# Performance work log

Hardware: AMD Instinct MI355X
Metric: run time of the kernel (lower is better)

## Reference

```python
import jax, jax.numpy as jnp
from jax import lax
import numpy as np

B, C, H, W = 2, 64, 128, 128
DN = ('NCHW', 'OIHW', 'NCHW')


def setup_inputs() -> dict:
    key = jax.random.key(0)
    ks = jax.random.split(key, 20)
    rn = lambda k, s, sc=0.05: jax.random.normal(k, s, dtype=jnp.float32) * sc
    inp = {
        'x': jax.random.normal(ks[0], (B, C, H, W), dtype=jnp.float32),
        'off1_w': rn(ks[1], (C, 1, 1, 15)), 'off1_b': rn(ks[2], (C,)),
        'bn1_s': 1.0 + rn(ks[3], (C,)), 'bn1_b': rn(ks[4], (C,)),
        'off2_w': rn(ks[5], (C, 1, 15, 1)), 'off2_b': rn(ks[6], (C,)),
        'bn2_s': 1.0 + rn(ks[7], (C,)), 'bn2_b': rn(ks[8], (C,)),
        'off3_w': rn(ks[9], (C, 1, 3, 3)), 'off3_b': rn(ks[10], (C,)),
        'bn3_s': 1.0 + rn(ks[11], (C,)), 'bn3_b': rn(ks[12], (C,)),
        'bal_w': rn(ks[13], (18, C, 1, 1)), 'bal_b': rn(ks[14], (18,)),
        'bn4_s': 1.0 + rn(ks[15], (18,)), 'bn4_b': rn(ks[16], (18,)),
        'dw2': rn(ks[17], (C, 1, 3, 3), 0.1),
        'dw3': rn(jax.random.fold_in(key, 101), (C, 1, 3, 3), 0.1),
        'dw4': rn(jax.random.fold_in(key, 102), (C, 1, 3, 3), 0.1),
        'dw5': rn(jax.random.fold_in(key, 103), (C, 1, 3, 3), 0.1),
        'fin_w': rn(ks[18], (C, C, 1, 1)), 'fin_b': rn(ks[19], (C,)),
        'bn5_s': 1.0 + rn(jax.random.fold_in(key, 104), (C,)),
        'bn5_b': rn(jax.random.fold_in(key, 105), (C,)),
    }
    return inp


def _dwconv(x, w, pad):
    return lax.conv_general_dilated(x, w, (1, 1), [(pad[0], pad[0]), (pad[1], pad[1])],
                                    dimension_numbers=DN, feature_group_count=x.shape[1])


def _conv1x1(x, w):
    return lax.conv_general_dilated(x, w, (1, 1), 'VALID', dimension_numbers=DN)


def _bias(x, b):
    return x + b[None, :, None, None]


def _bn(x, s, b):  # inference-form BatchNorm folded into per-channel affine
    return x * s[None, :, None, None] + b[None, :, None, None]


def _bilinear(x, py, px):
    # x: [B,C,H,W]; py/px: [B,9,H,W] float sampling coords -> [B,C,9,H,W]
    Bn, Cn, Hn, Wn = x.shape
    y0 = jnp.floor(py)
    x0 = jnp.floor(px)
    wy1 = py - y0  # fractional parts
    wx1 = px - x0
    xf = x.reshape(Bn, Cn, Hn * Wn)

    def gather(yi, xi):
        valid = (yi >= 0) & (yi <= Hn - 1) & (xi >= 0) & (xi <= Wn - 1)
        yc = jnp.clip(yi, 0, Hn - 1).astype(jnp.int32)
        xc = jnp.clip(xi, 0, Wn - 1).astype(jnp.int32)
        idx = (yc * Wn + xc).reshape(Bn, -1)  # [B, 9*H*W]
        v = jax.vmap(lambda f, i: f[:, i])(xf, idx)  # [B,C,9*H*W]
        v = v.reshape(Bn, Cn, 9, Hn, Wn)
        return v * valid[:, None].astype(x.dtype)  # zero padding outside

    g00 = gather(y0, x0)
    g01 = gather(y0, x0 + 1)
    g10 = gather(y0 + 1, x0)
    g11 = gather(y0 + 1, x0 + 1)
    wy1e = wy1[:, None]
    wx1e = wx1[:, None]
    return (g00 * (1 - wy1e) * (1 - wx1e) + g01 * (1 - wy1e) * wx1e
            + g10 * wy1e * (1 - wx1e) + g11 * wy1e * wx1e)


def _deform_dw(x, offsets, w, d):
    # depthwise DeformConv2d: kernel 3x3, stride 1, padding=d, dilation=d, groups=C
    Bn, Cn, Hn, Wn = x.shape
    off = offsets.reshape(Bn, 9, 2, Hn, Wn)  # pairs (dy, dx) per kernel tap, row-major
    ky = (jnp.arange(9) // 3 - 1).astype(x.dtype)  # [-1,-1,-1,0,0,0,1,1,1]
    kx = (jnp.arange(9) % 3 - 1).astype(x.dtype)
    hs = jnp.arange(Hn, dtype=x.dtype)
    ws = jnp.arange(Wn, dtype=x.dtype)
    # output loc h maps to input h - pad + ki*dil = h + (ki-1)*d since pad == dil == d
    py = off[:, :, 0] + (hs[:, None] + d * ky[:, None, None])[None]  # [B,9,H,W]
    px = off[:, :, 1] + (ws[None, :] + d * kx[:, None, None])[None]
    s = _bilinear(x, py, px)  # [B,C,9,H,W]
    return jnp.einsum('bckhw,ck->bchw', s, w.reshape(Cn, 9))


def reference(x, off1_w, off1_b, bn1_s, bn1_b, off2_w, off2_b, bn2_s, bn2_b,
              off3_w, off3_b, bn3_s, bn3_b, bal_w, bal_b, bn4_s, bn4_b,
              dw2, dw3, dw4, dw5, fin_w, fin_b, bn5_s, bn5_b):
    # DirectionOffsets: three depthwise convs + BN, summed, then 1x1 -> 18ch + BN
    o1 = _bn(_bias(_dwconv(x, off1_w, (0, 7)), off1_b), bn1_s, bn1_b)
    o2 = _bn(_bias(_dwconv(x, off2_w, (7, 0)), off2_b), bn2_s, bn2_b)
    o3 = _bn(_bias(_dwconv(x, off3_w, (1, 1)), off3_b), bn3_s, bn3_b)
    off = _bn(_bias(_conv1x1(o1 + o2 + o3, bal_w), bal_b), bn4_s, bn4_b)  # [B,18,H,W]
    # four deformable depthwise convs sharing the offset field
    out = (_deform_dw(x, off, dw2, 2) + _deform_dw(x, off, dw3, 3)
           + _deform_dw(x, off, dw4, 4) + _deform_dw(x, off, dw5, 5))
    out = _bn(_bias(_conv1x1(out, fin_w), fin_b), bn5_s, bn5_b) * x
    return out
```

## Files before the change

### kernel.cpp

```cpp
#include <hip/hip_runtime.h>

#define BB 2
#define CC 64
#define HH 128
#define WW 128
#define HWN (HH*WW)
#define CHW (CC*HWN)

#define BAND_H 8
#define HALO   8
#define NBAND  (HH / BAND_H)
#define LROWS  (BAND_H + 2 * HALO)
#define CPB    2
#define XPAD   8
#define XSTR   (WW + 2 * XPAD)

#define OB_H 16
#define OB_HALO 7
#define OB_ROWS (OB_H + 2 * OB_HALO)
#define OSTR 144

__global__ __launch_bounds__(256) void osum_kernel(const float* __restrict__ x,
    const float* __restrict__ w1, const float* __restrict__ b1, const float* __restrict__ s1, const float* __restrict__ g1,
    const float* __restrict__ w2, const float* __restrict__ b2, const float* __restrict__ s2, const float* __restrict__ g2,
    const float* __restrict__ w3, const float* __restrict__ b3, const float* __restrict__ s3, const float* __restrict__ g3,
    float* __restrict__ osum)
{
    __shared__ float xs[OB_ROWS * OSTR];
    int bid  = blockIdx.x;
    int band = bid & 7;
    int bc   = bid >> 3;
    int c    = bc & (CC - 1);
    int bs   = band * OB_H;
    int r_lo_v = bs - OB_HALO;

    for (int i = threadIdx.x; i < (OB_ROWS * OSTR) / 4; i += 256)
        ((float4*)xs)[i] = make_float4(0.f, 0.f, 0.f, 0.f);
    __syncthreads();

    int gstart = r_lo_v < 0 ? 0 : r_lo_v;
    int gend   = r_lo_v + OB_ROWS; if (gend > HH) gend = HH;
    int nitems = (gend - gstart) * (WW / 4);
    const float* xp = x + (size_t)bc * HWN;
    for (int i = threadIdx.x; i < nitems; i += 256) {
        int r = i >> 5, col4 = i & 31;
        int g = gstart + r;
        int lr = g - r_lo_v;
        ((float4*)xs)[lr * (OSTR / 4) + 2 + col4] = ((const float4*)(xp + g * WW))[col4];
    }
    __syncthreads();

    float W1[15], W2[15], W3[9];
    #pragma unroll
    for (int k = 0; k < 15; ++k) { W1[k] = w1[c * 15 + k]; W2[k] = w2[c * 15 + k]; }
    #pragma unroll
    for (int k = 0; k < 9; ++k) W3[k] = w3[c * 9 + k];
    float bb1 = b1[c], ss1 = s1[c], gg1 = g1[c];
    float bb2 = b2[c], ss2 = s2[c], gg2 = g2[c];
    float bb3 = b3[c], ss3 = s3[c], gg3 = g3[c];

    #pragma unroll
    for (int i = 0; i < (OB_H * WW) / 256; ++i) {
        int p = bs * WW + i * 256 + threadIdx.x;
        int h = p >> 7;
        int w = p & (WW - 1);
        int lr = h - r_lo_v;
        int base = lr * OSTR + XPAD + w;

        float a1 = 0.f;
        #pragma unroll
        for (int k = 0; k < 15; ++k) a1 += xs[base + k - 7] * W1[k];
        float a2 = 0.f;
        #pragma unroll
        for (int k = 0; k < 15; ++k) a2 += xs[base + (k - 7) * OSTR] * W2[k];
        float a3 = 0.f;
        #pragma unroll
        for (int kh = 0; kh < 3; ++kh)
            #pragma unroll
            for (int kw = 0; kw < 3; ++kw)
                a3 += xs[base + (kh - 1) * OSTR + (kw - 1)] * W3[kh * 3 + kw];

        osum[(size_t)bc * HWN + p] = (a1 + bb1) * ss1 + gg1
                                   + (a2 + bb2) * ss2 + gg2
                                   + (a3 + bb3) * ss3 + gg3;
    }
}

__global__ __launch_bounds__(256) void off_kernel(const float* __restrict__ osum,
    const float* __restrict__ balw, const float* __restrict__ balb,
    const float* __restrict__ s4, const float* __restrict__ g4,
    float* __restrict__ off)
{
    __shared__ float ls[CC * 128];
    int bid = blockIdx.x;
    int b   = bid >> 7;
    int hw0 = (bid & 127) * 128;

    const float* src = osum + (size_t)b * CHW + hw0;
    #pragma unroll
    for (int i = 0; i < 8; ++i) {
        int idx = threadIdx.x + i * 256;
        int row = idx >> 5, col4 = idx & 31;
        ((float4*)ls)[row * 32 + col4] = *(const float4*)(src + (size_t)row * HWN + col4 * 4);
    }
    __syncthreads();

    int hw = (threadIdx.x & 63) + ((threadIdx.x >> 6) & 1) * 64;
    int og = __builtin_amdgcn_readfirstlane((int)(threadIdx.x >> 7));

    float acc[9];
    #pragma unroll
    for (int j = 0; j < 9; ++j) acc[j] = 0.f;
    for (int ic = 0; ic < CC; ++ic) {
        float v = ls[ic * 128 + hw];
        #pragma unroll
        for (int j = 0; j < 9; ++j)
            acc[j] += v * balw[(og * 9 + j) * CC + ic];
    }
    #pragma unroll
    for (int j = 0; j < 9; ++j) {
        int oc = og * 9 + j;
        off[(size_t)b * (18 * HWN) + (size_t)oc * HWN + hw0 + hw] =
            (acc[j] + balb[oc]) * s4[oc] + g4[oc];
    }
}

__device__ __forceinline__ float gz(const float* __restrict__ xp, int y, int x) {
    return ((unsigned)y < (unsigned)HH && (unsigned)x < (unsigned)WW) ? xp[y * WW + x] : 0.f;
}

__global__ __launch_bounds__(256) void deform_kernel(
    const float* __restrict__ x,
    const float* __restrict__ off,
    const float* __restrict__ dw2, const float* __restrict__ dw3,
    const float* __restrict__ dw4, const float* __restrict__ dw5,
    float* __restrict__ pre)
{
    __shared__ float xs[LROWS * XSTR * CPB];

    int bid  = blockIdx.x;
    int band = bid & (NBAND - 1);
    int bcp  = bid >> 4;
    int cp   = bcp & 31;
    int b    = bcp >> 5;
    int c0   = cp * CPB;
    int bc0  = b * CC + c0;

    int r_lo_v = band * BAND_H - HALO;

    for (int i = threadIdx.x; i < (LROWS * XSTR * CPB) / 4; i += 256)
        ((float4*)xs)[i] = make_float4(0.f, 0.f, 0.f, 0.f);
    __syncthreads();

    int gstart = r_lo_v < 0 ? 0 : r_lo_v;
    int gend   = r_lo_v + LROWS; if (gend > HH) gend = HH;
    int nitems = (gend - gstart) * (WW / 4);
    const float* xp0 = x + (size_t)bc0 * HWN;
    const float* xp1 = xp0 + HWN;
    for (int i = threadIdx.x; i < nitems; i += 256) {
        int r = i >> 5, col4 = i & 31;
        int g = gstart + r;
        int lr = g - r_lo_v;
        float4 q0 = ((const float4*)(xp0 + g * WW))[col4];
        float4 q1 = ((const float4*)(xp1 + g * WW))[col4];
        ((float4*)xs)[lr * (XSTR / 2) + XPAD / 2 + col4 * 2]     = make_float4(q0.x, q1.x, q0.y, q1.y);
        ((float4*)xs)[lr * (XSTR / 2) + XPAD / 2 + col4 * 2 + 1] = make_float4(q0.z, q1.z, q0.w, q1.w);
    }
    __syncthreads();

    const float2* XS2 = (const float2*)xs;
    const float* offb = off + (size_t)b * (18 * HWN);

    #pragma unroll 1
    for (int chunk = 0; chunk < (BAND_H * WW) / 256; ++chunk) {
        int p = band * (BAND_H * WW) + chunk * 256 + (int)threadIdx.x;
        float hf = (float)(p >> 7);
        float wf = (float)(p & (WW - 1));

        float oy[9], ox[9];
        #pragma unroll
        for (int k = 0; k < 9; ++k) {
            oy[k] = offb[((size_t)(2 * k) << 14) + p];
            ox[k] = offb[((size_t)(2 * k + 1) << 14) + p];
        }

        float acc0 = 0.f, acc1 = 0.f;
        #pragma unroll
        for (int k = 0; k < 9; ++k) {
            const int ky = k / 3 - 1, kx = k % 3 - 1;
            float pyb = oy[k] + hf;
            float pxb = ox[k] + wf;
            float y0f = floorf(pyb), x0f = floorf(pxb);
            float wy = pyb - y0f, wx = pxb - x0f;
            int y0g = (int)y0f, x0g = (int)x0f;
            int y0b = y0g - r_lo_v;
            int x0b = x0g + XPAD;
            float cxa = 1.f - wx, cxb = wx;

            const int dkyLo = (ky < 0) ? -5 : (ky > 0 ? 2 : 0);
            const int dkyHi = (ky < 0) ? -2 : (ky > 0 ? 5 : 0);
            const int dkxLo = (kx < 0) ? -5 : (kx > 0 ? 2 : 0);
            const int dkxHi = (kx < 0) ? -2 : (kx > 0 ? 5 : 0);
            bool ok = (y0b + dkyLo >= 0) & (y0b + dkyHi <= LROWS - 2)
                    & (x0b + dkxLo >= 0) & (x0b + dkxHi <= XSTR - 2);

            if (ok) {
                #pragma unroll
                for (int di = 0; di < 4; ++di) {
                    const int d = di + 2;
                    int f0 = (y0b + d * ky) * XSTR + (x0b + d * kx);
                    float2 a  = XS2[f0],        bq = XS2[f0 + 1];
                    float2 cq = XS2[f0 + XSTR], dq = XS2[f0 + XSTR + 1];
                    float ra0 = cxa * a.x + cxb * bq.x;
                    float rb0 = cxa * cq.x + cxb * dq.x;
                    float ra1 = cxa * a.y + cxb * bq.y;
                    float rb1 = cxa * cq.y + cxb * dq.y;
                    float s0 = ra0 + wy * (rb0 - ra0);
                    float s1 = ra1 + wy * (rb1 - ra1);
                    const float* dwp = (di == 0) ? dw2 : (di == 1) ? dw3 : (di == 2) ? dw4 : dw5;
                    acc0 += s0 * dwp[c0 * 9 + k];
                    acc1 += s1 * dwp[(c0 + 1) * 9 + k];
                }
            } else {
                #pragma unroll
                for (int di = 0; di < 4; ++di) {
                    const int d = di + 2;
                    int yy = y0g + d * ky, xx = x0g + d * kx;
                    float v00 = gz(xp0, yy, xx),     v01 = gz(xp0, yy, xx + 1);
                    float v10 = gz(xp0, yy + 1, xx), v11 = gz(xp0, yy + 1, xx + 1);
                    float u00 = gz(xp1, yy, xx),     u01 = gz(xp1, yy, xx + 1);
                    float u10 = gz(xp1, yy + 1, xx), u11 = gz(xp1, yy + 1, xx + 1);
                    float s0 = (1.f - wy) * (cxa * v00 + cxb * v01) + wy * (cxa * v10 + cxb * v11);
                    float s1 = (1.f - wy) * (cxa * u00 + cxb * u01) + wy * (cxa * u10 + cxb * u11);
                    const float* dwp = (di == 0) ? dw2 : (di == 1) ? dw3 : (di == 2) ? dw4 : dw5;
                    acc0 += s0 * dwp[c0 * 9 + k];
                    acc1 += s1 * dwp[(c0 + 1) * 9 + k];
                }
            }
        }
        pre[((size_t)bc0 << 14) + p]       = acc0;
        pre[((size_t)(bc0 + 1) << 14) + p] = acc1;
    }
}

__global__ __launch_bounds__(256) void final_kernel(const float* __restrict__ pre,
    const float* __restrict__ finw, const float* __restrict__ finb,
    const float* __restrict__ s5, const float* __restrict__ g5,
    const float* __restrict__ x, float* __restrict__ out)
{
    __shared__ float ls[CC * 64];
    int bid = blockIdx.x;
    int b   = bid >> 8;
    int hw0 = (bid & 255) * 64;

    const float* src = pre + (size_t)b * CHW + hw0;
    #pragma unroll
    for (int i = 0; i < 4; ++i) {
        int idx = threadIdx.x + i * 256;
        int row = idx >> 4, col4 = idx & 15;
        ((float4*)ls)[row * 16 + col4] = *(const float4*)(src + (size_t)row * HWN + col4 * 4);
    }
    __syncthreads();

    int hw = threadIdx.x & 63;
    int og = __builtin_amdgcn_readfirstlane((int)(threadIdx.x >> 6));

    float acc[16];
    #pragma unroll
    for (int j = 0; j < 16; ++j) acc[j] = 0.f;
    for (int ic = 0; ic < CC; ++ic) {
        float v = ls[ic * 64 + hw];
        #pragma unroll
        for (int j = 0; j < 16; ++j)
            acc[j] += v * finw[(og * 16 + j) * CC + ic];
    }
    #pragma unroll
    for (int j = 0; j < 16; ++j) {
        int oc = og * 16 + j;
        size_t oidx = ((size_t)(b * CC + oc) << 14) + hw0 + hw;
        out[oidx] = ((acc[j] + finb[oc]) * s5[oc] + g5[oc]) * x[oidx];
    }
}

extern "C" void kernel_launch(void* const* d_in, const int* in_sizes, int n_in,
                              void* d_out, int out_size, void* d_ws, size_t ws_size,
                              hipStream_t stream) {
    const float* x      = (const float*)d_in[0];
    const float* off1_w = (const float*)d_in[1];
    const float* off1_b = (const float*)d_in[2];
    const float* bn1_s  = (const float*)d_in[3];
    const float* bn1_b  = (const float*)d_in[4];
    const float* off2_w = (const float*)d_in[5];
    const float* off2_b = (const float*)d_in[6];
    const float* bn2_s  = (const float*)d_in[7];
    const float* bn2_b  = (const float*)d_in[8];
    const float* off3_w = (const float*)d_in[9];
    const float* off3_b = (const float*)d_in[10];
    const float* bn3_s  = (const float*)d_in[11];
    const float* bn3_b  = (const float*)d_in[12];
    const float* bal_w  = (const float*)d_in[13];
    const float* bal_b  = (const float*)d_in[14];
    const float* bn4_s  = (const float*)d_in[15];
    const float* bn4_b  = (const float*)d_in[16];
    const float* dw2    = (const float*)d_in[17];
    const float* dw3    = (const float*)d_in[18];
    const float* dw4    = (const float*)d_in[19];
    const float* dw5    = (const float*)d_in[20];
    const float* fin_w  = (const float*)d_in[21];
    const float* fin_b  = (const float*)d_in[22];
    const float* bn5_s  = (const float*)d_in[23];
    const float* bn5_b  = (const float*)d_in[24];

    float* ws   = (float*)d_ws;
    float* osum = ws;
    float* off  = ws + (size_t)BB * CHW;
    float* pre  = off + (size_t)BB * 18 * HWN;

    float* out = (float*)d_out;

    osum_kernel<<<BB * CC * (HH / OB_H), 256, 0, stream>>>(x,
        off1_w, off1_b, bn1_s, bn1_b,
        off2_w, off2_b, bn2_s, bn2_b,
        off3_w, off3_b, bn3_s, bn3_b, osum);
    off_kernel<<<BB * (HWN / 128), 256, 0, stream>>>(osum, bal_w, bal_b, bn4_s, bn4_b, off);
    deform_kernel<<<BB * (CC / CPB) * NBAND, 256, 0, stream>>>(x, off, dw2, dw3, dw4, dw5, pre);
    final_kernel<<<BB * (HWN / 64), 256, 0, stream>>>(pre, fin_w, fin_b, bn5_s, bn5_b, x, out);
}
```

Before: 162.6 us.

## Process four channels per block and share bilinear taps across dilations

The deformable depthwise kernel now handles four channels per block, with an interleaved float4 LDS layout, so each offset read and each address computation serves four channels instead of two. For the centre tap, where all four dilations sample the same location, the four weights are pre-summed and a single bilinear sample is taken. For axis-aligned taps, the overlapping samples along a row or column are loaded once into a 5-entry register window and reused across dilations. HALO drops to 7 and launch bounds request 3 blocks per SIMD. Costs are half as many blocks, higher register pressure, and larger LDS per block.

```diff
diff --git a/kernel.cpp b/kernel.cpp
--- a/kernel.cpp
+++ b/kernel.cpp
@@ -8,10 +8,10 @@
 #define CHW (CC*HWN)
 
 #define BAND_H 8
-#define HALO   8
+#define HALO   7
 #define NBAND  (HH / BAND_H)
 #define LROWS  (BAND_H + 2 * HALO)
-#define CPB    2
+#define CPB    4
 #define XPAD   8
 #define XSTR   (WW + 2 * XPAD)
 
@@ -129,27 +129,50 @@
     return ((unsigned)y < (unsigned)HH && (unsigned)x < (unsigned)WW) ? xp[y * WW + x] : 0.f;
 }
 
-__global__ __launch_bounds__(256) void deform_kernel(
+__device__ __forceinline__ float bil_g(const float* __restrict__ xp, int yy, int xx,
+                                       float cxa, float cxb, float wy) {
+    float v00 = gz(xp, yy, xx),     v01 = gz(xp, yy, xx + 1);
+    float v10 = gz(xp, yy + 1, xx), v11 = gz(xp, yy + 1, xx + 1);
+    float ra = cxa * v00 + cxb * v01;
+    float rb = cxa * v10 + cxb * v11;
+    return ra + wy * (rb - ra);
+}
+
+__device__ __forceinline__ void bl4(const float4 a, const float4 b, const float4 c, const float4 d,
+                                    float cxa, float cxb, float wy,
+                                    float w0, float w1, float w2, float w3,
+                                    float (&acc)[4])
+{
+    float ra, rb, s;
+    ra = cxa * a.x + cxb * b.x; rb = cxa * c.x + cxb * d.x; s = ra + wy * (rb - ra); acc[0] += s * w0;
+    ra = cxa * a.y + cxb * b.y; rb = cxa * c.y + cxb * d.y; s = ra + wy * (rb - ra); acc[1] += s * w1;
+    ra = cxa * a.z + cxb * b.z; rb = cxa * c.z + cxb * d.z; s = ra + wy * (rb - ra); acc[2] += s * w2;
+    ra = cxa * a.w + cxb * b.w; rb = cxa * c.w + cxb * d.w; s = ra + wy * (rb - ra); acc[3] += s * w3;
+}
+
+#define DWP(di) ((di) == 0 ? dw2 : (di) == 1 ? dw3 : (di) == 2 ? dw4 : dw5)
+
+__global__ __launch_bounds__(256, 3) void deform_kernel(
     const float* __restrict__ x,
     const float* __restrict__ off,
     const float* __restrict__ dw2, const float* __restrict__ dw3,
     const float* __restrict__ dw4, const float* __restrict__ dw5,
     float* __restrict__ pre)
 {
-    __shared__ float xs[LROWS * XSTR * CPB];
+    __shared__ float4 xs4[LROWS * XSTR];
 
     int bid  = blockIdx.x;
     int band = bid & (NBAND - 1);
     int bcp  = bid >> 4;
-    int cp   = bcp & 31;
-    int b    = bcp >> 5;
+    int cp   = bcp & (CC / CPB - 1);
+    int b    = bcp >> 4;
     int c0   = cp * CPB;
     int bc0  = b * CC + c0;
 
     int r_lo_v = band * BAND_H - HALO;
 
-    for (int i = threadIdx.x; i < (LROWS * XSTR * CPB) / 4; i += 256)
-        ((float4*)xs)[i] = make_float4(0.f, 0.f, 0.f, 0.f);
+    for (int i = threadIdx.x; i < LROWS * XSTR; i += 256)
+        xs4[i] = make_float4(0.f, 0.f, 0.f, 0.f);
     __syncthreads();
 
     int gstart = r_lo_v < 0 ? 0 : r_lo_v;
@@ -157,19 +180,33 @@
     int nitems = (gend - gstart) * (WW / 4);
     const float* xp0 = x + (size_t)bc0 * HWN;
     const float* xp1 = xp0 + HWN;
+    const float* xp2 = xp1 + HWN;
+    const float* xp3 = xp2 + HWN;
     for (int i = threadIdx.x; i < nitems; i += 256) {
         int r = i >> 5, col4 = i & 31;
         int g = gstart + r;
         int lr = g - r_lo_v;
         float4 q0 = ((const float4*)(xp0 + g * WW))[col4];
         float4 q1 = ((const float4*)(xp1 + g * WW))[col4];
-        ((float4*)xs)[lr * (XSTR / 2) + XPAD / 2 + col4 * 2]     = make_float4(q0.x, q1.x, q0.y, q1.y);
-        ((float4*)xs)[lr * (XSTR / 2) + XPAD / 2 + col4 * 2 + 1] = make_float4(q0.z, q1.z, q0.w, q1.w);
-    }
-    __syncthreads();
-
-    const float2* XS2 = (const float2*)xs;
+        float4 q2 = ((const float4*)(xp2 + g * WW))[col4];
+        float4 q3 = ((const float4*)(xp3 + g * WW))[col4];
+        float4* dst = &xs4[lr * XSTR + XPAD + col4 * 4];
+        dst[0] = make_float4(q0.x, q1.x, q2.x, q3.x);
+        dst[1] = make_float4(q0.y, q1.y, q2.y, q3.y);
+        dst[2] = make_float4(q0.z, q1.z, q2.z, q3.z);
+        dst[3] = make_float4(q0.w, q1.w, q2.w, q3.w);
+    }
+    __syncthreads();
+
+    const float4* XS4 = xs4;
     const float* offb = off + (size_t)b * (18 * HWN);
+    const float* xpc[4] = { xp0, xp1, xp2, xp3 };
+
+    float wc[4];
+    #pragma unroll
+    for (int j = 0; j < 4; ++j)
+        wc[j] = dw2[(c0 + j) * 9 + 4] + dw3[(c0 + j) * 9 + 4]
+              + dw4[(c0 + j) * 9 + 4] + dw5[(c0 + j) * 9 + 4];
 
     #pragma unroll 1
     for (int chunk = 0; chunk < (BAND_H * WW) / 256; ++chunk) {
@@ -184,7 +221,7 @@
             ox[k] = offb[((size_t)(2 * k + 1) << 14) + p];
         }
 
-        float acc0 = 0.f, acc1 = 0.f;
+        float acc[4] = {0.f, 0.f, 0.f, 0.f};
         #pragma unroll
         for (int k = 0; k < 9; ++k) {
             const int ky = k / 3 - 1, kx = k % 3 - 1;
@@ -205,41 +242,75 @@
                     & (x0b + dkxLo >= 0) & (x0b + dkxHi <= XSTR - 2);
 
             if (ok) {
-                #pragma unroll
-                for (int di = 0; di < 4; ++di) {
-                    const int d = di + 2;
-                    int f0 = (y0b + d * ky) * XSTR + (x0b + d * kx);
-                    float2 a  = XS2[f0],        bq = XS2[f0 + 1];
-                    float2 cq = XS2[f0 + XSTR], dq = XS2[f0 + XSTR + 1];
-                    float ra0 = cxa * a.x + cxb * bq.x;
-                    float rb0 = cxa * cq.x + cxb * dq.x;
-                    float ra1 = cxa * a.y + cxb * bq.y;
-                    float rb1 = cxa * cq.y + cxb * dq.y;
-                    float s0 = ra0 + wy * (rb0 - ra0);
-                    float s1 = ra1 + wy * (rb1 - ra1);
-                    const float* dwp = (di == 0) ? dw2 : (di == 1) ? dw3 : (di == 2) ? dw4 : dw5;
-                    acc0 += s0 * dwp[c0 * 9 + k];
-                    acc1 += s1 * dwp[(c0 + 1) * 9 + k];
+                if (ky == 0 && kx == 0) {
+                    int f0 = y0b * XSTR + x0b;
+                    float4 a = XS4[f0],        bq = XS4[f0 + 1];
+                    float4 cq = XS4[f0 + XSTR], dq = XS4[f0 + XSTR + 1];
+                    bl4(a, bq, cq, dq, cxa, cxb, wy, wc[0], wc[1], wc[2], wc[3], acc);
+                } else if (ky == 0) {
+                    int cbase = x0b + (kx < 0 ? -5 : 2);
+                    int f0 = y0b * XSTR + cbase, f1 = f0 + XSTR;
+                    float4 top[5], bot[5];
+                    #pragma unroll
+                    for (int j = 0; j < 5; ++j) { top[j] = XS4[f0 + j]; bot[j] = XS4[f1 + j]; }
+                    #pragma unroll
+                    for (int di = 0; di < 4; ++di) {
+                        const int jj = (kx < 0) ? (3 - di) : di;
+                        const float* dwp = DWP(di);
+                        bl4(top[jj], top[jj + 1], bot[jj], bot[jj + 1], cxa, cxb, wy,
+                            dwp[(c0 + 0) * 9 + k], dwp[(c0 + 1) * 9 + k],
+                            dwp[(c0 + 2) * 9 + k], dwp[(c0 + 3) * 9 + k], acc);
+                    }
+                } else if (kx == 0) {
+                    int rbase = y0b + (ky < 0 ? -5 : 2);
+                    float4 L[5], R[5];
+                    #pragma unroll
+                    for (int j = 0; j < 5; ++j) {
+                        int f = (rbase + j) * XSTR + x0b;
+                        L[j] = XS4[f]; R[j] = XS4[f + 1];
+                    }
+                    #pragma unroll
+                    for (int di = 0; di < 4; ++di) {
+                        const int jj = (ky < 0) ? (3 - di) : di;
+                        const float* dwp = DWP(di);
+                        bl4(L[jj], R[jj], L[jj + 1], R[jj + 1], cxa, cxb, wy,
+                            dwp[(c0 + 0) * 9 + k], dwp[(c0 + 1) * 9 + k],
+                            dwp[(c0 + 2) * 9 + k], dwp[(c0 + 3) * 9 + k], acc);
+                    }
+                } else {
+                    #pragma unroll
+                    for (int di = 0; di < 4; ++di) {
+                        const int d = di + 2;
+                        int f0 = (y0b + d * ky) * XSTR + (x0b + d * kx);
+                        float4 a = XS4[f0],        bq = XS4[f0 + 1];
+                        float4 cq = XS4[f0 + XSTR], dq = XS4[f0 + XSTR + 1];
+                        const float* dwp = DWP(di);
+                        bl4(a, bq, cq, dq, cxa, cxb, wy,
+                            dwp[(c0 + 0) * 9 + k], dwp[(c0 + 1) * 9 + k],
+                            dwp[(c0 + 2) * 9 + k], dwp[(c0 + 3) * 9 + k], acc);
+                    }
                 }
             } else {
-                #pragma unroll
-                for (int di = 0; di < 4; ++di) {
-                    const int d = di + 2;
-                    int yy = y0g + d * ky, xx = x0g + d * kx;
-                    float v00 = gz(xp0, yy, xx),     v01 = gz(xp0, yy, xx + 1);
-                    float v10 = gz(xp0, yy + 1, xx), v11 = gz(xp0, yy + 1, xx + 1);
-                    float u00 = gz(xp1, yy, xx),     u01 = gz(xp1, yy, xx + 1);
-                    float u10 = gz(xp1, yy + 1, xx), u11 = gz(xp1, yy + 1, xx + 1);
-                    float s0 = (1.f - wy) * (cxa * v00 + cxb * v01) + wy * (cxa * v10 + cxb * v11);
-                    float s1 = (1.f - wy) * (cxa * u00 + cxb * u01) + wy * (cxa * u10 + cxb * u11);
-                    const float* dwp = (di == 0) ? dw2 : (di == 1) ? dw3 : (di == 2) ? dw4 : dw5;
-                    acc0 += s0 * dwp[c0 * 9 + k];
-                    acc1 += s1 * dwp[(c0 + 1) * 9 + k];
+                if (ky == 0 && kx == 0) {
+                    #pragma unroll
+                    for (int j = 0; j < 4; ++j)
+                        acc[j] += bil_g(xpc[j], y0g, x0g, cxa, cxb, wy) * wc[j];
+                } else {
+                    #pragma unroll
+                    for (int di = 0; di < 4; ++di) {
+                        const int d = di + 2;
+                        int yy = y0g + d * ky, xx = x0g + d * kx;
+                        const float* dwp = DWP(di);
+                        #pragma unroll
+                        for (int j = 0; j < 4; ++j)
+                            acc[j] += bil_g(xpc[j], yy, xx, cxa, cxb, wy) * dwp[(c0 + j) * 9 + k];
+                    }
                 }
             }
         }
-        pre[((size_t)bc0 << 14) + p]       = acc0;
-        pre[((size_t)(bc0 + 1) << 14) + p] = acc1;
+        #pragma unroll
+        for (int j = 0; j < 4; ++j)
+            pre[((size_t)(bc0 + j) << 14) + p] = acc[j];
     }
 }
 
```

New measurement: 161.0 us. No clear change (-1.0%).
